# Performance work log

Hardware: AMD Instinct MI355X
Metric: run time of the kernel (lower is better)

The kernel has to match this reference:

```python
import jax, jax.numpy as jnp
import numpy as np

B, T, IN, HID = 256, 512, 1024, 1024


def setup_inputs() -> dict:
    key = jax.random.key(0)
    ks = jax.random.split(key, 9)
    s = 1.0 / np.sqrt(IN + HID)
    def lin(k):
        kw, kb = jax.random.split(k)
        W = jax.random.uniform(kw, (IN + HID, HID), jnp.float32, -s, s)
        b = jax.random.uniform(kb, (HID,), jnp.float32, -s, s)
        return W, b
    Wf, bf = lin(ks[0])
    Wi, bi = lin(ks[1])
    Wo, bo = lin(ks[2])
    Wc, bc = lin(ks[3])
    x = jax.random.normal(ks[4], (B, T, IN), jnp.float32)
    return {"x": x, "Wf": Wf, "bf": bf, "Wi": Wi, "bi": bi,
            "Wo": Wo, "bo": bo, "Wc": Wc, "bc": bc}


def reference(x, Wf, bf, Wi, bi, Wo, bo, Wc, bc):
    # x: [B, T, IN]; returns final (h, c): each [B, HID]
    batch = x.shape[0]
    hid = Wf.shape[1]

    def step(carry, xt):
        h, c = carry
        comb = jnp.concatenate([xt, h], axis=1)      # [B, IN+HID]
        i = jax.nn.sigmoid(comb @ Wi + bi)
        f = jax.nn.sigmoid(comb @ Wf + bf)
        o = jax.nn.sigmoid(comb @ Wo + bo)
        g = jnp.tanh(comb @ Wc + bc)
        c_next = f * c + i * g
        h_next = o * jnp.tanh(c_next)
        return (h_next, c_next), None

    init = (jnp.zeros((batch, hid), x.dtype), jnp.zeros((batch, hid), x.dtype))
    (h, c), _ = jax.lax.scan(step, init, jnp.swapaxes(x, 0, 1))
    return (h, c)
```

## Files before the change

### kernel.cpp

```cpp
#include <hip/hip_runtime.h>
#include <hip/hip_bf16.h>

#define B_DIM 256
#define T_DIM 512
#define WINT 32
#define NWIN 16
#define IN_DIM 1024
#define HID_DIM 1024
#define BLK 16384

typedef __attribute__((ext_vector_type(8))) short bf16x8;
typedef __attribute__((ext_vector_type(4))) float f32x4;

__device__ __forceinline__ unsigned short f2bf(float v) {
  unsigned int u = __float_as_uint(v);
  unsigned int r = (u + 0x7fffu + ((u >> 16) & 1u)) >> 16;
  return (unsigned short)r;
}
__device__ __forceinline__ float bflo(unsigned u) { return __uint_as_float(u << 16); }
__device__ __forceinline__ float bfhi(unsigned u) { return __uint_as_float(u & 0xffff0000u); }

typedef __attribute__((address_space(3))) unsigned int lds_uint;
typedef const __attribute__((address_space(1))) unsigned int g_uint;
__device__ __forceinline__ void gload_lds16(const void* g, void* l) {
  __builtin_amdgcn_global_load_lds((g_uint*)g, (lds_uint*)l, 16, 0, 0);
}
__device__ __forceinline__ void glds2(const unsigned char* s, unsigned char* d) {
  gload_lds16(s, d);
  gload_lds16(s + 1024, d + 1024);
}

#define WAITVM(N) asm volatile("s_waitcnt vmcnt(" #N ")" ::: "memory")

__global__ void prep_pack_w(const float* __restrict__ Wi, const float* __restrict__ Wf,
                            const float* __restrict__ Wo, const float* __restrict__ Wc,
                            unsigned char* __restrict__ Wp) {
  const int bid = blockIdx.x;
  const int cb = bid >> 4, kc = bid & 15;
  const int tid = threadIdx.x;
  const int col = tid & 63;
  const int g = col >> 4, h_in = col & 15;
  const int kq = tid >> 6;
  const float* W = (g == 0) ? Wi : (g == 1) ? Wf : (g == 2) ? Wo : Wc;
  const float* src = W + (size_t)(kc * 128 + kq * 32) * HID_DIM + cb * 16 + h_in;
  unsigned char* dst = Wp + (size_t)bid * BLK;
  const unsigned int xo = (unsigned int)((col & 7) << 4);
#pragma unroll
  for (int b4 = 0; b4 < 4; ++b4) {
    unsigned short u[8];
#pragma unroll
    for (int j = 0; j < 8; ++j)
      u[j] = f2bf(src[(size_t)(b4 * 8 + j) * HID_DIM]);
    uint4 pk;
    pk.x = (unsigned)u[0] | ((unsigned)u[1] << 16);
    pk.y = (unsigned)u[2] | ((unsigned)u[3] << 16);
    pk.z = (unsigned)u[4] | ((unsigned)u[5] << 16);
    pk.w = (unsigned)u[6] | ((unsigned)u[7] << 16);
    unsigned int byte = ((unsigned int)(col * 256 + kq * 64 + b4 * 16)) ^ xo;
    *(uint4*)(dst + byte) = pk;
  }
}

__global__ void prep_bias(const float* __restrict__ bi, const float* __restrict__ bf_,
                          const float* __restrict__ bo, const float* __restrict__ bc,
                          float* __restrict__ bp) {
  int p = blockIdx.x * 256 + threadIdx.x;
  int cbb = p >> 6, col = p & 63, g = col >> 4, h_in = col & 15;
  const float* b = (g == 0) ? bi : (g == 1) ? bf_ : (g == 2) ? bo : bc;
  bp[p] = b[cbb * 16 + h_in];
}

__global__ void prep_pack_x_win(const float* __restrict__ x,
                                unsigned char* __restrict__ xpw, int t0) {
  const int bid = blockIdx.x;
  const int kc = bid & 7, mb = (bid >> 3) & 3, tw = bid >> 5;
  const int tid = threadIdx.x;
  const int row = tid >> 2, kseg = tid & 3;
  const float* src = x + ((size_t)(mb * 64 + row) * T_DIM + (t0 + tw)) * IN_DIM +
                     kc * 128 + kseg * 32;
  unsigned char* dst = xpw + (size_t)bid * BLK;
  const unsigned int xo = (unsigned)((row & 7) << 4);
#pragma unroll
  for (int c4 = 0; c4 < 4; ++c4) {
    float4 f0 = *(const float4*)(src + c4 * 8);
    float4 f1 = *(const float4*)(src + c4 * 8 + 4);
    uint4 pk;
    pk.x = (unsigned)f2bf(f0.x) | ((unsigned)f2bf(f0.y) << 16);
    pk.y = (unsigned)f2bf(f0.z) | ((unsigned)f2bf(f0.w) << 16);
    pk.z = (unsigned)f2bf(f1.x) | ((unsigned)f2bf(f1.y) << 16);
    pk.w = (unsigned)f2bf(f1.z) | ((unsigned)f2bf(f1.w) << 16);
    *(uint4*)(dst + (((unsigned)(row * 256 + kseg * 64 + c4 * 16)) ^ xo)) = pk;
  }
}

__global__ __launch_bounds__(512, 2) void lstm_fused(
    const unsigned char* __restrict__ gxCur, const unsigned char* __restrict__ xpNext,
    const unsigned char* __restrict__ Wq, const float* __restrict__ bp,
    unsigned char* __restrict__ gxNext, unsigned char* hring,
    unsigned int* flags, float* cst, float* __restrict__ out,
    int t0, int mode) {
  extern __shared__ unsigned char ring[];
  const int tid = threadIdx.x, lane = tid & 63, w = tid >> 6;
  const int cg = w & 3, kh = w >> 2;
  const int fr = lane & 15;
  const unsigned koff2 = (unsigned)((lane >> 4) << 4);
  const int rsub = (lane >> 4) * 4;
  const int cl = cg * 16 + fr;

  bool isSeq; int wg;
  if (mode == 0) {
    isSeq = (int)blockIdx.x < 256;
    wg = isSeq ? (int)blockIdx.x : (int)blockIdx.x - 256;
  } else {
    isSeq = (mode == 1);
    wg = (int)blockIdx.x;
  }
  const int mb = (wg >> 6) & 3, cb = wg & 63;

  bf16x8 Breg[4][4];
  {
    const int xoff = isSeq ? 8 : 0;
#pragma unroll
    for (int kcl = 0; kcl < 4; ++kcl)
#pragma unroll
      for (int ks = 0; ks < 4; ++ks)
        Breg[kcl][ks] = *(const bf16x8*)(
            Wq + ((size_t)(cb * 16 + xoff + kh * 4 + kcl) << 14) +
            (((unsigned)cl * 256 + (unsigned)ks * 64 + koff2) ^
             ((unsigned)((cl & 7) << 4))));
#pragma unroll
    for (int kcl = 0; kcl < 4; ++kcl)
#pragma unroll
      for (int ks = 0; ks < 4; ++ks)
        asm volatile("" : "+v"(Breg[kcl][ks]));
  }

  float* gates0 = (float*)ring;
  float* gates1 = (float*)(ring + 32768);

  auto phases = [&](const unsigned char* Abase, f32x4* acc) {
#pragma unroll
    for (int c = 0; c < 4; ++c)
      glds2(Abase + (size_t)c * BLK, ring + c * 16384 + w * 2048);
#pragma unroll
    for (int kc = 0; kc < 8; ++kc) {
      if (kc <= 4) WAITVM(6);
      else if (kc == 5) WAITVM(4);
      else if (kc == 6) WAITVM(2);
      else WAITVM(0);
      __builtin_amdgcn_s_barrier();
      if ((kc >> 2) == kh) {
        const int kcl = kc & 3;
        const unsigned char* Ab = ring + (kc & 3) * 16384;
#pragma unroll
        for (int ks = 0; ks < 4; ++ks) {
          const unsigned kb = (unsigned)ks * 64 + koff2;
#pragma unroll
          for (int rb = 0; rb < 4; ++rb) {
            const unsigned r0 = (unsigned)(rb * 16 + fr);
            bf16x8 a0 = *(const bf16x8*)(Ab + ((r0 * 256 + kb) ^ ((r0 & 7) << 4)));
            acc[rb] = __builtin_amdgcn_mfma_f32_16x16x32_bf16(
                a0, Breg[kcl][ks], acc[rb], 0, 0, 0);
          }
        }
      }
      __builtin_amdgcn_s_barrier();
      if (kc + 4 < 8)
        glds2(Abase + (size_t)(kc + 4) * BLK, ring + (kc & 3) * 16384 + w * 2048);
    }
  };

  if (isSeq) {
    const int erow = tid & 63, hb2 = (tid >> 6) * 2;
    const size_t gidx = (size_t)(mb * 64 + erow) * HID_DIM + cb * 16 + hb2;
    float bI[2], bF[2], bO[2], bG[2];
#pragma unroll
    for (int j = 0; j < 2; ++j) {
      bI[j] = bp[cb * 64 + hb2 + j];
      bF[j] = bp[cb * 64 + 16 + hb2 + j];
      bO[j] = bp[cb * 64 + 32 + hb2 + j];
      bG[j] = bp[cb * 64 + 48 + hb2 + j];
    }
    float cr[2] = {0.f, 0.f};
    if (t0 > 0) { float2 c2v = *(const float2*)(cst + gidx); cr[0] = c2v.x; cr[1] = c2v.y; }

#pragma unroll 1
    for (int tt = 0; tt < WINT; ++tt) {
      const int t = t0 + tt;
#pragma unroll
      for (int kcl = 0; kcl < 4; ++kcl)
#pragma unroll
        for (int ks = 0; ks < 4; ++ks)
          asm volatile("" : "+v"(Breg[kcl][ks]));
      uint4 gxv = *(const uint4*)(gxCur + ((size_t)((tt * 4 + mb) * 64 + cb)) * 8192 +
                                  (size_t)tid * 16);
      f32x4 acc[4] = {{0.f,0.f,0.f,0.f},{0.f,0.f,0.f,0.f},
                      {0.f,0.f,0.f,0.f},{0.f,0.f,0.f,0.f}};
      if (t > 0) {
        if (w == 0) {
          unsigned int* fl = &flags[mb * 64 + lane];
          while (!__all(__hip_atomic_load(fl, __ATOMIC_RELAXED,
                                          __HIP_MEMORY_SCOPE_AGENT) >= (unsigned)t))
            __builtin_amdgcn_s_sleep(2);
          (void)__hip_atomic_load(fl, __ATOMIC_ACQUIRE,
                                  __HIP_MEMORY_SCOPE_AGENT);
        }
        __syncthreads();
        const unsigned char* hA = hring + (size_t)((t + 2) % 3) * 524288 +
                                  (size_t)(mb * 8) * BLK + w * 2048 + lane * 16;
        phases(hA, acc);
      }
      {
        float* g_ = kh ? gates1 : gates0;
#pragma unroll
        for (int rb = 0; rb < 4; ++rb)
#pragma unroll
          for (int j = 0; j < 4; ++j)
            g_[(rb * 16 + rsub + j) * 65 + cg * 16 + fr] = acc[rb][j];
      }
      __syncthreads();
      float hv[2];
      {
        unsigned gu0 = gxv.x, gu1 = gxv.y, gu2 = gxv.z, gu3 = gxv.w;
#pragma unroll
        for (int j = 0; j < 2; ++j) {
          int hc = hb2 + j;
          float gx0 = j ? bfhi(gu0) : bflo(gu0);
          float gx1 = j ? bfhi(gu1) : bflo(gu1);
          float gx2 = j ? bfhi(gu2) : bflo(gu2);
          float gx3 = j ? bfhi(gu3) : bflo(gu3);
          float pi = gates0[erow * 65 + hc]      + gates1[erow * 65 + hc]      + bI[j] + gx0;
          float pf = gates0[erow * 65 + 16 + hc] + gates1[erow * 65 + 16 + hc] + bF[j] + gx1;
          float po = gates0[erow * 65 + 32 + hc] + gates1[erow * 65 + 32 + hc] + bO[j] + gx2;
          float pg = gates0[erow * 65 + 48 + hc] + gates1[erow * 65 + 48 + hc] + bG[j] + gx3;
          float ig = 1.f / (1.f + __expf(-pi));
          float fg = 1.f / (1.f + __expf(-pf));
          float og = 1.f / (1.f + __expf(-po));
          float gg = 1.f - 2.f / (1.f + __expf(2.f * pg));
          float cn = fg * cr[j] + ig * gg;
          cr[j] = cn;
          hv[j] = og * (1.f - 2.f / (1.f + __expf(2.f * cn)));
        }
      }
      if (t < T_DIM - 1) {
        int hcg = cb * 16 + hb2;
        int kc2 = hcg >> 7, kp = hcg & 127;
        unsigned byte = ((unsigned)(erow * 256 + kp * 2)) ^ ((unsigned)((erow & 7) << 4));
        unsigned pk = (unsigned)f2bf(hv[0]) | ((unsigned)f2bf(hv[1]) << 16);
        unsigned int* hd = (unsigned int*)(hring + (size_t)(t % 3) * 524288 +
                                           (size_t)(mb * 8 + kc2) * BLK + byte);
        __hip_atomic_store(hd, pk, __ATOMIC_RELAXED, __HIP_MEMORY_SCOPE_AGENT);
      }
      WAITVM(0);
      __syncthreads();
      if (tid == 0 && t < T_DIM - 1)
        __hip_atomic_store(&flags[mb * 64 + cb], (unsigned)(t + 1),
                           __ATOMIC_RELEASE, __HIP_MEMORY_SCOPE_AGENT);
      if (t == T_DIM - 1) {
        *(float2*)(out + gidx) = make_float2(hv[0], hv[1]);
        *(float2*)(out + (size_t)B_DIM * HID_DIM + gidx) = make_float2(cr[0], cr[1]);
      }
    }
    if (t0 + WINT < T_DIM) *(float2*)(cst + gidx) = make_float2(cr[0], cr[1]);
  } else {
    const int erow = tid & 63, hb2 = (tid >> 6) * 2;
#pragma unroll 1
    for (int tl = 0; tl < WINT; ++tl) {
#pragma unroll
      for (int kcl = 0; kcl < 4; ++kcl)
#pragma unroll
        for (int ks = 0; ks < 4; ++ks)
          asm volatile("" : "+v"(Breg[kcl][ks]));
      f32x4 acc[4] = {{0.f,0.f,0.f,0.f},{0.f,0.f,0.f,0.f},
                      {0.f,0.f,0.f,0.f},{0.f,0.f,0.f,0.f}};
      const unsigned char* xA = xpNext + ((size_t)((tl * 4 + mb) * 8)) * BLK +
                                w * 2048 + lane * 16;
      phases(xA, acc);
      {
        float* g_ = kh ? gates1 : gates0;
#pragma unroll
        for (int rb = 0; rb < 4; ++rb)
#pragma unroll
          for (int j = 0; j < 4; ++j)
            g_[(rb * 16 + rsub + j) * 65 + cg * 16 + fr] = acc[rb][j];
      }
      __syncthreads();
      {
        unsigned u[4];
#pragma unroll
        for (int g = 0; g < 4; ++g) {
          float lo = gates0[erow * 65 + g * 16 + hb2] + gates1[erow * 65 + g * 16 + hb2];
          float hi = gates0[erow * 65 + g * 16 + hb2 + 1] + gates1[erow * 65 + g * 16 + hb2 + 1];
          u[g] = (unsigned)f2bf(lo) | ((unsigned)f2bf(hi) << 16);
        }
        uint4 pk; pk.x = u[0]; pk.y = u[1]; pk.z = u[2]; pk.w = u[3];
        *(uint4*)(gxNext + ((size_t)((tl * 4 + mb) * 64 + cb)) * 8192 +
                  (size_t)tid * 16) = pk;
      }
      __syncthreads();
    }
  }
}

extern "C" void kernel_launch(void* const* d_in, const int* in_sizes, int n_in,
                              void* d_out, int out_size, void* d_ws, size_t ws_size,
                              hipStream_t stream) {
  (void)in_sizes; (void)n_in; (void)out_size;
  const float* x   = (const float*)d_in[0];
  const float* Wf_ = (const float*)d_in[1];
  const float* bf_ = (const float*)d_in[2];
  const float* Wi_ = (const float*)d_in[3];
  const float* bi_ = (const float*)d_in[4];
  const float* Wo_ = (const float*)d_in[5];
  const float* bo_ = (const float*)d_in[6];
  const float* Wc_ = (const float*)d_in[7];
  const float* bc_ = (const float*)d_in[8];
  float* out = (float*)d_out;
  unsigned char* ws = (unsigned char*)d_ws;

  unsigned char* Wp = ws;
  size_t off = 16777216;
  float* bp = (float*)(ws + off);                    off += 16384;
  unsigned int* flags = (unsigned int*)(ws + off);   off += 8192;
  off += 8192;
  unsigned char* hring = ws + off;                   off += 3 * 524288;
  float* cst = (float*)(ws + off);                   off += 1048576;
  unsigned char* xpw0 = ws + off;                    off += (size_t)WINT * 32 * BLK;
  unsigned char* xpw1 = ws + off;                    off += (size_t)WINT * 32 * BLK;
  unsigned char* gxw0 = ws + off;                    off += (size_t)WINT * 256 * 8192;
  unsigned char* gxw1 = ws + off;                    off += (size_t)WINT * 256 * 8192;
  if (ws_size < off) return;

  prep_pack_w<<<1024, 256, 0, stream>>>(Wi_, Wf_, Wo_, Wc_, Wp);
  prep_bias<<<16, 256, 0, stream>>>(bi_, bf_, bo_, bc_, bp);
  hipMemsetAsync(flags, 0, 8192, stream);

  hipFuncSetAttribute((const void*)lstm_fused,
                      hipFuncAttributeMaxDynamicSharedMemorySize, 65536);
  int nb = 0;
  hipOccupancyMaxActiveBlocksPerMultiprocessor(&nb, (const void*)lstm_fused, 512, 65536);
  const bool canFuse = (nb >= 2);

  prep_pack_x_win<<<WINT * 32, 256, 0, stream>>>(x, xpw0, 0);
  {
    const unsigned char* a_gc = gxw1;
    const unsigned char* a_xp = xpw0;
    const unsigned char* a_wp = Wp;
    const float* a_bp = bp;
    unsigned char* a_gn = gxw0;
    lstm_fused<<<256, 512, 65536, stream>>>(a_gc, a_xp, a_wp, a_bp, a_gn, hring,
                                            flags, cst, out, 0, 2);
  }

  for (int wnd = 0; wnd < NWIN; ++wnd) {
    const int t0v = wnd * WINT;
    unsigned char* gxC = (wnd & 1) ? gxw1 : gxw0;
    unsigned char* gxN = (wnd & 1) ? gxw0 : gxw1;
    unsigned char* xpN = (wnd & 1) ? xpw0 : xpw1;
    if (wnd < NWIN - 1)
      prep_pack_x_win<<<WINT * 32, 256, 0, stream>>>(x, xpN, (wnd + 1) * WINT);

    const unsigned char* a_gc = gxC;
    const unsigned char* a_xp = xpN;
    const unsigned char* a_wp = Wp;
    const float* a_bp = bp;
    unsigned char* a_gn = gxN;
    unsigned char* a_hr = hring;
    unsigned int* a_fl = flags;
    float* a_cs = cst;
    float* a_out = out;
    int a_t0 = t0v;

    if (canFuse && wnd < NWIN - 1) {
      int a_mode = 0;
      void* args[] = {&a_gc, &a_xp, &a_wp, &a_bp, &a_gn, &a_hr, &a_fl, &a_cs,
                      &a_out, &a_t0, &a_mode};
      hipLaunchCooperativeKernel((const void*)lstm_fused, dim3(512), dim3(512),
                                 args, 65536u, stream);
    } else {
      int a_mode = 1;
      void* args[] = {&a_gc, &a_xp, &a_wp, &a_bp, &a_gn, &a_hr, &a_fl, &a_cs,
                      &a_out, &a_t0, &a_mode};
      hipLaunchCooperativeKernel((const void*)lstm_fused, dim3(256), dim3(512),
                                 args, 65536u, stream);
      if (wnd < NWIN - 1)
        lstm_fused<<<256, 512, 65536, stream>>>(a_gc, a_xp, a_wp, a_bp, a_gn,
                                                a_hr, a_fl, a_cs, a_out, a_t0, 2);
    }
  }
}
```

Before: 9.900 ms.

## Fuse input projection into single persistent LSTM kernel, removing windowed launches

Replaces the windowed scheme (separate x-packing kernels, per-window cooperative launches with seq/bulk block roles, and a global gx buffer in bf16) with one persistent cooperative kernel of 256 blocks. Each block holds both recurrent and input weight slices in registers, converts x to bf16 into LDS itself, and computes the next step's input gates before each recurrent step, keeping them in fp32 registers. This is meant to remove launch overhead and gx/xp global round trips, but it puts the input GEMM on the serial critical path of every step and doubles register and LDS use per block (occupancy 1, 128KB LDS).

```diff
diff --git a/kernel.cpp b/kernel.cpp
--- a/kernel.cpp
+++ b/kernel.cpp
@@ -3,8 +3,6 @@
 
 #define B_DIM 256
 #define T_DIM 512
-#define WINT 32
-#define NWIN 16
 #define IN_DIM 1024
 #define HID_DIM 1024
 #define BLK 16384
@@ -17,8 +15,6 @@
   unsigned int r = (u + 0x7fffu + ((u >> 16) & 1u)) >> 16;
   return (unsigned short)r;
 }
-__device__ __forceinline__ float bflo(unsigned u) { return __uint_as_float(u << 16); }
-__device__ __forceinline__ float bfhi(unsigned u) { return __uint_as_float(u & 0xffff0000u); }
 
 typedef __attribute__((address_space(3))) unsigned int lds_uint;
 typedef const __attribute__((address_space(1))) unsigned int g_uint;
@@ -70,78 +66,88 @@
   bp[p] = b[cbb * 16 + h_in];
 }
 
-__global__ void prep_pack_x_win(const float* __restrict__ x,
-                                unsigned char* __restrict__ xpw, int t0) {
-  const int bid = blockIdx.x;
-  const int kc = bid & 7, mb = (bid >> 3) & 3, tw = bid >> 5;
-  const int tid = threadIdx.x;
-  const int row = tid >> 2, kseg = tid & 3;
-  const float* src = x + ((size_t)(mb * 64 + row) * T_DIM + (t0 + tw)) * IN_DIM +
-                     kc * 128 + kseg * 32;
-  unsigned char* dst = xpw + (size_t)bid * BLK;
-  const unsigned int xo = (unsigned)((row & 7) << 4);
-#pragma unroll
-  for (int c4 = 0; c4 < 4; ++c4) {
-    float4 f0 = *(const float4*)(src + c4 * 8);
-    float4 f1 = *(const float4*)(src + c4 * 8 + 4);
-    uint4 pk;
-    pk.x = (unsigned)f2bf(f0.x) | ((unsigned)f2bf(f0.y) << 16);
-    pk.y = (unsigned)f2bf(f0.z) | ((unsigned)f2bf(f0.w) << 16);
-    pk.z = (unsigned)f2bf(f1.x) | ((unsigned)f2bf(f1.y) << 16);
-    pk.w = (unsigned)f2bf(f1.z) | ((unsigned)f2bf(f1.w) << 16);
-    *(uint4*)(dst + (((unsigned)(row * 256 + kseg * 64 + c4 * 16)) ^ xo)) = pk;
-  }
-}
-
-__global__ __launch_bounds__(512, 2) void lstm_fused(
-    const unsigned char* __restrict__ gxCur, const unsigned char* __restrict__ xpNext,
-    const unsigned char* __restrict__ Wq, const float* __restrict__ bp,
-    unsigned char* __restrict__ gxNext, unsigned char* hring,
-    unsigned int* flags, float* cst, float* __restrict__ out,
-    int t0, int mode) {
+__global__ __launch_bounds__(512, 1) void lstm_one(
+    const float* __restrict__ x, const unsigned char* __restrict__ Wq,
+    const float* __restrict__ bp, unsigned char* hring,
+    unsigned int* flags, float* __restrict__ out) {
   extern __shared__ unsigned char ring[];
+  unsigned char* seqring = ring;
+  unsigned char* bulkring = ring + 65536;
+  const int wg = blockIdx.x, mb = wg >> 6, cb = wg & 63;
   const int tid = threadIdx.x, lane = tid & 63, w = tid >> 6;
   const int cg = w & 3, kh = w >> 2;
   const int fr = lane & 15;
   const unsigned koff2 = (unsigned)((lane >> 4) << 4);
   const int rsub = (lane >> 4) * 4;
   const int cl = cg * 16 + fr;
-
-  bool isSeq; int wg;
-  if (mode == 0) {
-    isSeq = (int)blockIdx.x < 256;
-    wg = isSeq ? (int)blockIdx.x : (int)blockIdx.x - 256;
-  } else {
-    isSeq = (mode == 1);
-    wg = (int)blockIdx.x;
+  const int srow = tid >> 3;
+  const int s32 = (tid & 7) * 32;
+
+  bf16x8 BregH[4][4], BregX[4][4];
+#pragma unroll
+  for (int kcl = 0; kcl < 4; ++kcl)
+#pragma unroll
+    for (int ks = 0; ks < 4; ++ks) {
+      const unsigned sw = (((unsigned)cl * 256 + (unsigned)ks * 64 + koff2) ^
+                           ((unsigned)((cl & 7) << 4)));
+      BregH[kcl][ks] = *(const bf16x8*)(
+          Wq + ((size_t)(cb * 16 + 8 + kh * 4 + kcl) << 14) + sw);
+      BregX[kcl][ks] = *(const bf16x8*)(
+          Wq + ((size_t)(cb * 16 + kh * 4 + kcl) << 14) + sw);
+    }
+#pragma unroll
+  for (int kcl = 0; kcl < 4; ++kcl)
+#pragma unroll
+    for (int ks = 0; ks < 4; ++ks) {
+      asm volatile("" : "+v"(BregH[kcl][ks]));
+      asm volatile("" : "+v"(BregX[kcl][ks]));
+    }
+
+  const int erow = tid & 63, hb2 = (tid >> 6) * 2;
+  const size_t gidx = (size_t)(mb * 64 + erow) * HID_DIM + cb * 16 + hb2;
+  float bI[2], bF[2], bO[2], bG[2];
+#pragma unroll
+  for (int j = 0; j < 2; ++j) {
+    bI[j] = bp[cb * 64 + hb2 + j];
+    bF[j] = bp[cb * 64 + 16 + hb2 + j];
+    bO[j] = bp[cb * 64 + 32 + hb2 + j];
+    bG[j] = bp[cb * 64 + 48 + hb2 + j];
   }
-  const int mb = (wg >> 6) & 3, cb = wg & 63;
-
-  bf16x8 Breg[4][4];
-  {
-    const int xoff = isSeq ? 8 : 0;
-#pragma unroll
-    for (int kcl = 0; kcl < 4; ++kcl)
-#pragma unroll
-      for (int ks = 0; ks < 4; ++ks)
-        Breg[kcl][ks] = *(const bf16x8*)(
-            Wq + ((size_t)(cb * 16 + xoff + kh * 4 + kcl) << 14) +
-            (((unsigned)cl * 256 + (unsigned)ks * 64 + koff2) ^
-             ((unsigned)((cl & 7) << 4))));
-#pragma unroll
-    for (int kcl = 0; kcl < 4; ++kcl)
-#pragma unroll
-      for (int ks = 0; ks < 4; ++ks)
-        asm volatile("" : "+v"(Breg[kcl][ks]));
-  }
-
-  float* gates0 = (float*)ring;
-  float* gates1 = (float*)(ring + 32768);
+  float cr[2] = {0.f, 0.f};
+  float gxv[8], gxn[8];
+#pragma unroll
+  for (int i = 0; i < 8; ++i) gxv[i] = 0.f;
+
+  float* gates0 = (float*)seqring;
+  float* gates1 = (float*)(seqring + 32768);
+  float* gatesB0 = (float*)bulkring;
+  float* gatesB1 = (float*)(bulkring + 32768);
+
+  auto stage_pair = [&](int t1, int p) {
+    const float* src = x + ((size_t)(mb * 64 + srow) * T_DIM + t1) * IN_DIM +
+                       p * 256 + s32;
+    unsigned char* dbuf = bulkring + (p & 1) * 32768;
+    const unsigned swz = (unsigned)((srow & 7) << 4);
+#pragma unroll
+    for (int c4 = 0; c4 < 4; ++c4) {
+      float4 f0 = *(const float4*)(src + c4 * 8);
+      float4 f1 = *(const float4*)(src + c4 * 8 + 4);
+      unsigned kk = (unsigned)(s32 + c4 * 8);
+      unsigned byte = ((kk >> 7) * 16384u) +
+                      ((((unsigned)srow * 256u + (kk & 127u) * 2u)) ^ swz);
+      uint4 pk;
+      pk.x = (unsigned)f2bf(f0.x) | ((unsigned)f2bf(f0.y) << 16);
+      pk.y = (unsigned)f2bf(f0.z) | ((unsigned)f2bf(f0.w) << 16);
+      pk.z = (unsigned)f2bf(f1.x) | ((unsigned)f2bf(f1.y) << 16);
+      pk.w = (unsigned)f2bf(f1.z) | ((unsigned)f2bf(f1.w) << 16);
+      *(uint4*)(dbuf + byte) = pk;
+    }
+  };
 
   auto phases = [&](const unsigned char* Abase, f32x4* acc) {
 #pragma unroll
     for (int c = 0; c < 4; ++c)
-      glds2(Abase + (size_t)c * BLK, ring + c * 16384 + w * 2048);
+      glds2(Abase + (size_t)c * BLK, seqring + c * 16384 + w * 2048);
 #pragma unroll
     for (int kc = 0; kc < 8; ++kc) {
       if (kc <= 4) WAITVM(6);
@@ -151,7 +157,7 @@
       __builtin_amdgcn_s_barrier();
       if ((kc >> 2) == kh) {
         const int kcl = kc & 3;
-        const unsigned char* Ab = ring + (kc & 3) * 16384;
+        const unsigned char* Ab = seqring + (kc & 3) * 16384;
 #pragma unroll
         for (int ks = 0; ks < 4; ++ks) {
           const unsigned kb = (unsigned)ks * 64 + koff2;
@@ -160,40 +166,75 @@
             const unsigned r0 = (unsigned)(rb * 16 + fr);
             bf16x8 a0 = *(const bf16x8*)(Ab + ((r0 * 256 + kb) ^ ((r0 & 7) << 4)));
             acc[rb] = __builtin_amdgcn_mfma_f32_16x16x32_bf16(
-                a0, Breg[kcl][ks], acc[rb], 0, 0, 0);
+                a0, BregH[kcl][ks], acc[rb], 0, 0, 0);
           }
         }
       }
       __builtin_amdgcn_s_barrier();
       if (kc + 4 < 8)
-        glds2(Abase + (size_t)(kc + 4) * BLK, ring + (kc & 3) * 16384 + w * 2048);
+        glds2(Abase + (size_t)(kc + 4) * BLK, seqring + (kc & 3) * 16384 + w * 2048);
     }
   };
 
-  if (isSeq) {
-    const int erow = tid & 63, hb2 = (tid >> 6) * 2;
-    const size_t gidx = (size_t)(mb * 64 + erow) * HID_DIM + cb * 16 + hb2;
-    float bI[2], bF[2], bO[2], bG[2];
-#pragma unroll
-    for (int j = 0; j < 2; ++j) {
-      bI[j] = bp[cb * 64 + hb2 + j];
-      bF[j] = bp[cb * 64 + 16 + hb2 + j];
-      bO[j] = bp[cb * 64 + 32 + hb2 + j];
-      bG[j] = bp[cb * 64 + 48 + hb2 + j];
-    }
-    float cr[2] = {0.f, 0.f};
-    if (t0 > 0) { float2 c2v = *(const float2*)(cst + gidx); cr[0] = c2v.x; cr[1] = c2v.y; }
-
 #pragma unroll 1
-    for (int tt = 0; tt < WINT; ++tt) {
-      const int t = t0 + tt;
-#pragma unroll
-      for (int kcl = 0; kcl < 4; ++kcl)
-#pragma unroll
-        for (int ks = 0; ks < 4; ++ks)
-          asm volatile("" : "+v"(Breg[kcl][ks]));
-      uint4 gxv = *(const uint4*)(gxCur + ((size_t)((tt * 4 + mb) * 64 + cb)) * 8192 +
-                                  (size_t)tid * 16);
+  for (int t = -1; t < T_DIM; ++t) {
+#pragma unroll
+    for (int kcl = 0; kcl < 4; ++kcl)
+#pragma unroll
+      for (int ks = 0; ks < 4; ++ks) {
+        asm volatile("" : "+v"(BregH[kcl][ks]));
+        asm volatile("" : "+v"(BregX[kcl][ks]));
+      }
+
+    const bool bulkAct = (t < T_DIM - 1);
+    if (bulkAct) {
+      f32x4 accB[4] = {{0.f,0.f,0.f,0.f},{0.f,0.f,0.f,0.f},
+                       {0.f,0.f,0.f,0.f},{0.f,0.f,0.f,0.f}};
+      stage_pair(t + 1, 0);
+      __syncthreads();
+#pragma unroll
+      for (int p = 0; p < 4; ++p) {
+        if (p < 3) stage_pair(t + 1, p + 1);
+#pragma unroll
+        for (int ci = 0; ci < 2; ++ci) {
+          const int c = p * 2 + ci;
+          if ((c >> 2) == kh) {
+            const int kcl = c & 3;
+            const unsigned char* Ab = bulkring + (p & 1) * 32768 + ci * 16384;
+#pragma unroll
+            for (int ks = 0; ks < 4; ++ks) {
+              const unsigned kb = (unsigned)ks * 64 + koff2;
+#pragma unroll
+              for (int rb = 0; rb < 4; ++rb) {
+                const unsigned r0 = (unsigned)(rb * 16 + fr);
+                bf16x8 a0 = *(const bf16x8*)(Ab + ((r0 * 256 + kb) ^ ((r0 & 7) << 4)));
+                accB[rb] = __builtin_amdgcn_mfma_f32_16x16x32_bf16(
+                    a0, BregX[kcl][ks], accB[rb], 0, 0, 0);
+              }
+            }
+          }
+        }
+        __syncthreads();
+      }
+      {
+        float* g_ = kh ? gatesB1 : gatesB0;
+#pragma unroll
+        for (int rb = 0; rb < 4; ++rb)
+#pragma unroll
+          for (int j = 0; j < 4; ++j)
+            g_[(rb * 16 + rsub + j) * 65 + cg * 16 + fr] = accB[rb][j];
+      }
+      __syncthreads();
+#pragma unroll
+      for (int g = 0; g < 4; ++g)
+#pragma unroll
+        for (int j = 0; j < 2; ++j)
+          gxn[g * 2 + j] = gatesB0[erow * 65 + g * 16 + hb2 + j] +
+                           gatesB1[erow * 65 + g * 16 + hb2 + j];
+      __syncthreads();
+    }
+
+    if (t >= 0) {
       f32x4 acc[4] = {{0.f,0.f,0.f,0.f},{0.f,0.f,0.f,0.f},
                       {0.f,0.f,0.f,0.f},{0.f,0.f,0.f,0.f}};
       if (t > 0) {
@@ -220,27 +261,20 @@
       }
       __syncthreads();
       float hv[2];
-      {
-        unsigned gu0 = gxv.x, gu1 = gxv.y, gu2 = gxv.z, gu3 = gxv.w;
-#pragma unroll
-        for (int j = 0; j < 2; ++j) {
-          int hc = hb2 + j;
-          float gx0 = j ? bfhi(gu0) : bflo(gu0);
-          float gx1 = j ? bfhi(gu1) : bflo(gu1);
-          float gx2 = j ? bfhi(gu2) : bflo(gu2);
-          float gx3 = j ? bfhi(gu3) : bflo(gu3);
-          float pi = gates0[erow * 65 + hc]      + gates1[erow * 65 + hc]      + bI[j] + gx0;
-          float pf = gates0[erow * 65 + 16 + hc] + gates1[erow * 65 + 16 + hc] + bF[j] + gx1;
-          float po = gates0[erow * 65 + 32 + hc] + gates1[erow * 65 + 32 + hc] + bO[j] + gx2;
-          float pg = gates0[erow * 65 + 48 + hc] + gates1[erow * 65 + 48 + hc] + bG[j] + gx3;
-          float ig = 1.f / (1.f + __expf(-pi));
-          float fg = 1.f / (1.f + __expf(-pf));
-          float og = 1.f / (1.f + __expf(-po));
-          float gg = 1.f - 2.f / (1.f + __expf(2.f * pg));
-          float cn = fg * cr[j] + ig * gg;
-          cr[j] = cn;
-          hv[j] = og * (1.f - 2.f / (1.f + __expf(2.f * cn)));
-        }
+#pragma unroll
+      for (int j = 0; j < 2; ++j) {
+        int hc = hb2 + j;
+        float pi = gates0[erow * 65 + hc]      + gates1[erow * 65 + hc]      + bI[j] + gxv[0 + j];
+        float pf = gates0[erow * 65 + 16 + hc] + gates1[erow * 65 + 16 + hc] + bF[j] + gxv[2 + j];
+        float po = gates0[erow * 65 + 32 + hc] + gates1[erow * 65 + 32 + hc] + bO[j] + gxv[4 + j];
+        float pg = gates0[erow * 65 + 48 + hc] + gates1[erow * 65 + 48 + hc] + bG[j] + gxv[6 + j];
+        float ig = 1.f / (1.f + __expf(-pi));
+        float fg = 1.f / (1.f + __expf(-pf));
+        float og = 1.f / (1.f + __expf(-po));
+        float gg = 1.f - 2.f / (1.f + __expf(2.f * pg));
+        float cn = fg * cr[j] + ig * gg;
+        cr[j] = cn;
+        hv[j] = og * (1.f - 2.f / (1.f + __expf(2.f * cn)));
       }
       if (t < T_DIM - 1) {
         int hcg = cb * 16 + hb2;
@@ -261,44 +295,8 @@
         *(float2*)(out + (size_t)B_DIM * HID_DIM + gidx) = make_float2(cr[0], cr[1]);
       }
     }
-    if (t0 + WINT < T_DIM) *(float2*)(cst + gidx) = make_float2(cr[0], cr[1]);
-  } else {
-    const int erow = tid & 63, hb2 = (tid >> 6) * 2;
-#pragma unroll 1
-    for (int tl = 0; tl < WINT; ++tl) {
-#pragma unroll
-      for (int kcl = 0; kcl < 4; ++kcl)
-#pragma unroll
-        for (int ks = 0; ks < 4; ++ks)
-          asm volatile("" : "+v"(Breg[kcl][ks]));
-      f32x4 acc[4] = {{0.f,0.f,0.f,0.f},{0.f,0.f,0.f,0.f},
-                      {0.f,0.f,0.f,0.f},{0.f,0.f,0.f,0.f}};
-      const unsigned char* xA = xpNext + ((size_t)((tl * 4 + mb) * 8)) * BLK +
-                                w * 2048 + lane * 16;
-      phases(xA, acc);
-      {
-        float* g_ = kh ? gates1 : gates0;
-#pragma unroll
-        for (int rb = 0; rb < 4; ++rb)
-#pragma unroll
-          for (int j = 0; j < 4; ++j)
-            g_[(rb * 16 + rsub + j) * 65 + cg * 16 + fr] = acc[rb][j];
-      }
-      __syncthreads();
-      {
-        unsigned u[4];
-#pragma unroll
-        for (int g = 0; g < 4; ++g) {
-          float lo = gates0[erow * 65 + g * 16 + hb2] + gates1[erow * 65 + g * 16 + hb2];
-          float hi = gates0[erow * 65 + g * 16 + hb2 + 1] + gates1[erow * 65 + g * 16 + hb2 + 1];
-          u[g] = (unsigned)f2bf(lo) | ((unsigned)f2bf(hi) << 16);
-        }
-        uint4 pk; pk.x = u[0]; pk.y = u[1]; pk.z = u[2]; pk.w = u[3];
-        *(uint4*)(gxNext + ((size_t)((tl * 4 + mb) * 64 + cb)) * 8192 +
-                  (size_t)tid * 16) = pk;
-      }
-      __syncthreads();
-    }
+#pragma unroll
+    for (int i = 0; i < 8; ++i) gxv[i] = gxn[i];
   }
 }
 
@@ -324,68 +322,21 @@
   unsigned int* flags = (unsigned int*)(ws + off);   off += 8192;
   off += 8192;
   unsigned char* hring = ws + off;                   off += 3 * 524288;
-  float* cst = (float*)(ws + off);                   off += 1048576;
-  unsigned char* xpw0 = ws + off;                    off += (size_t)WINT * 32 * BLK;
-  unsigned char* xpw1 = ws + off;                    off += (size_t)WINT * 32 * BLK;
-  unsigned char* gxw0 = ws + off;                    off += (size_t)WINT * 256 * 8192;
-  unsigned char* gxw1 = ws + off;                    off += (size_t)WINT * 256 * 8192;
   if (ws_size < off) return;
 
   prep_pack_w<<<1024, 256, 0, stream>>>(Wi_, Wf_, Wo_, Wc_, Wp);
   prep_bias<<<16, 256, 0, stream>>>(bi_, bf_, bo_, bc_, bp);
   hipMemsetAsync(flags, 0, 8192, stream);
 
-  hipFuncSetAttribute((const void*)lstm_fused,
-                      hipFuncAttributeMaxDynamicSharedMemorySize, 65536);
-  int nb = 0;
-  hipOccupancyMaxActiveBlocksPerMultiprocessor(&nb, (const void*)lstm_fused, 512, 65536);
-  const bool canFuse = (nb >= 2);
-
-  prep_pack_x_win<<<WINT * 32, 256, 0, stream>>>(x, xpw0, 0);
-  {
-    const unsigned char* a_gc = gxw1;
-    const unsigned char* a_xp = xpw0;
-    const unsigned char* a_wp = Wp;
-    const float* a_bp = bp;
-    unsigned char* a_gn = gxw0;
-    lstm_fused<<<256, 512, 65536, stream>>>(a_gc, a_xp, a_wp, a_bp, a_gn, hring,
-                                            flags, cst, out, 0, 2);
-  }
-
-  for (int wnd = 0; wnd < NWIN; ++wnd) {
-    const int t0v = wnd * WINT;
-    unsigned char* gxC = (wnd & 1) ? gxw1 : gxw0;
-    unsigned char* gxN = (wnd & 1) ? gxw0 : gxw1;
-    unsigned char* xpN = (wnd & 1) ? xpw0 : xpw1;
-    if (wnd < NWIN - 1)
-      prep_pack_x_win<<<WINT * 32, 256, 0, stream>>>(x, xpN, (wnd + 1) * WINT);
-
-    const unsigned char* a_gc = gxC;
-    const unsigned char* a_xp = xpN;
-    const unsigned char* a_wp = Wp;
-    const float* a_bp = bp;
-    unsigned char* a_gn = gxN;
-    unsigned char* a_hr = hring;
-    unsigned int* a_fl = flags;
-    float* a_cs = cst;
-    float* a_out = out;
-    int a_t0 = t0v;
-
-    if (canFuse && wnd < NWIN - 1) {
-      int a_mode = 0;
-      void* args[] = {&a_gc, &a_xp, &a_wp, &a_bp, &a_gn, &a_hr, &a_fl, &a_cs,
-                      &a_out, &a_t0, &a_mode};
-      hipLaunchCooperativeKernel((const void*)lstm_fused, dim3(512), dim3(512),
-                                 args, 65536u, stream);
-    } else {
-      int a_mode = 1;
-      void* args[] = {&a_gc, &a_xp, &a_wp, &a_bp, &a_gn, &a_hr, &a_fl, &a_cs,
-                      &a_out, &a_t0, &a_mode};
-      hipLaunchCooperativeKernel((const void*)lstm_fused, dim3(256), dim3(512),
-                                 args, 65536u, stream);
-      if (wnd < NWIN - 1)
-        lstm_fused<<<256, 512, 65536, stream>>>(a_gc, a_xp, a_wp, a_bp, a_gn,
-                                                a_hr, a_fl, a_cs, a_out, a_t0, 2);
-    }
-  }
-}
+  hipFuncSetAttribute((const void*)lstm_one,
+                      hipFuncAttributeMaxDynamicSharedMemorySize, 131072);
+  const float* a_x = x;
+  const unsigned char* a_wp = Wp;
+  const float* a_bp = bp;
+  unsigned char* a_hr = hring;
+  unsigned int* a_fl = flags;
+  float* a_out = out;
+  void* args[] = {&a_x, &a_wp, &a_bp, &a_hr, &a_fl, &a_out};
+  hipLaunchCooperativeKernel((const void*)lstm_one, dim3(256), dim3(512),
+                             args, 131072u, stream);
+}
```

Result: slower. 14.39 ms (+45.4%).
